# Kernel optimization log

Hardware: AMD Instinct MI355X
Metric: run time of the kernel (lower is better)

The kernel has to match this reference:

```python
import jax, jax.numpy as jnp
import numpy as np
from jax import lax

WORD_NUM = 30000
EMBED = 128
RNN = 256
CLASSES = 9
BATCH = 128
SEQ = 512


def setup_inputs() -> dict:
    key = jax.random.key(0)
    ks = jax.random.split(key, 7)
    s_e = 1.0 / np.sqrt(EMBED)
    s_r = 1.0 / np.sqrt(RNN)
    return {
        "input_x": jax.random.randint(ks[0], (BATCH, SEQ), 0, WORD_NUM, dtype=jnp.int32),
        "embed": jax.random.normal(ks[1], (WORD_NUM, EMBED), dtype=jnp.float32) * 0.05,
        # LSTM kernel/recurrent kernel, gate order i|f|g|o (Keras convention)
        "W": jax.random.normal(ks[2], (EMBED, 4 * RNN), dtype=jnp.float32) * s_e,
        "U": jax.random.normal(ks[3], (RNN, 4 * RNN), dtype=jnp.float32) * s_r,
        "b": jnp.zeros((4 * RNN,), dtype=jnp.float32),
        "Wout": jax.random.normal(ks[4], (RNN, CLASSES), dtype=jnp.float32) * s_r,
        "bout": jnp.zeros((CLASSES,), dtype=jnp.float32),
    }


def _lstm(xs, W, U, b, h0, c0):
    # xs: [T, B, E] -> hidden sequence [T, B, R], final (h, c)
    def step(carry, x):
        h, c = carry
        z = x @ W + h @ U + b  # [B, 4R]
        i, f, g, o = jnp.split(z, 4, axis=-1)
        i = jax.nn.sigmoid(i)
        f = jax.nn.sigmoid(f)
        g = jnp.tanh(g)
        o = jax.nn.sigmoid(o)
        c = f * c + i * g
        h = o * jnp.tanh(c)
        return (h, c), h

    (h, c), hs = lax.scan(step, (h0, c0), xs)
    return hs, h, c


def reference(input_x, embed, W, U, b, Wout, bout):
    # Embedding lookup: [B, S] -> [B, S, E]
    x = embed[input_x]
    B = x.shape[0]
    R = U.shape[0]
    h0 = jnp.zeros((B, R), dtype=x.dtype)
    c0 = jnp.zeros((B, R), dtype=x.dtype)
    xs = jnp.swapaxes(x, 0, 1)  # [S, B, E] for time-major scan
    hs, h_last, c_last = _lstm(xs, W, U, b, h0, c0)
    hs = jnp.swapaxes(hs, 0, 1)  # [B, S, R]
    probs = jax.nn.softmax(hs @ Wout + bout, axis=-1)  # [B, S, C]
    # Keras return_state -> (sequence_output, last_h, last_c); state=(hc, hs)
    return probs, (h_last, c_last)
```

## Files before the change

### kernel.cpp

```cpp
#include <hip/hip_runtime.h>
#include <math.h>

#define B 128
#define S 512
#define E 128
#define R 256

#define NG 32
#define QW 8
#define ELS 4
#define OUTS 128
#define UNITS 32

typedef float v2f __attribute__((ext_vector_type(2)));

static const size_t HX_OFF   = 0;
static const size_t XG_OFF   = HX_OFF + 2ull * B * R;
static const size_t WUT_OFF  = XG_OFF + (size_t)S * B * E;
static const size_t SYNC_OFF = WUT_OFF + 1024ull * 384;
static const size_t WS_FLOATS = SYNC_OFF + 1024;

#define HOUT_OFF 589824
#define COUT_OFF 622592

__global__ void zero_sync(int* __restrict__ sync) {
    sync[threadIdx.x] = 0;
}

__global__ void gather_x(const int* __restrict__ idx, const float* __restrict__ embed,
                         float* __restrict__ Xg) {
    int t    = blockIdx.x;
    int tid  = threadIdx.x;
    int b    = tid >> 1;
    int half = tid & 1;
    int row  = idx[(size_t)b * S + t];
    const float4* er = (const float4*)(embed + (size_t)row * E) + half * 16;
    float4* xw = (float4*)(Xg + ((size_t)t * B + b) * E) + half * 16;
#pragma unroll
    for (int k = 0; k < 16; ++k) xw[k] = er[k];
}

__global__ void make_wut(const float* __restrict__ W, const float* __restrict__ U,
                         float* __restrict__ WUt) {
    int j = blockIdx.x;
    int s = threadIdx.x;
    float v = (s < E) ? W[(size_t)s * 1024 + j] : U[(size_t)(s - E) * 1024 + j];
    WUt[(size_t)j * 384 + s] = v;
}

__device__ __forceinline__ float sigm(float x) { return 1.f / (1.f + __expf(-x)); }

__launch_bounds__(512, 2)
__global__ void lstm_persist(const float* __restrict__ Xg, const float* __restrict__ WUt,
                             const float* __restrict__ bias, const float* __restrict__ Wout,
                             const float* __restrict__ bout, float* __restrict__ out,
                             float* __restrict__ HX, int* __restrict__ sync) {
    __shared__ float act[ELS][E + R];
    __shared__ float partial[4][ELS][OUTS];
    __shared__ float woutT[9][260];
    __shared__ float zrow[ELS][12];

    const int tid  = threadIdx.x;
    const int wg   = blockIdx.x;
    const int g    = wg >> 3;
    const int q    = wg & 7;
    const int lane = tid & 63;
    const int wv   = __builtin_amdgcn_readfirstlane(tid >> 6);
    const int ks   = wv >> 1;
    const int oi   = ((wv & 1) << 6) | lane;
    const int j    = (oi >> 5) * 256 + q * 32 + (oi & 31);

    float4 wx[8], wh[16];
    {
        const float4* wrow = (const float4*)(WUt + (size_t)j * 384);
#pragma unroll
        for (int p = 0; p < 8; ++p)  wx[p] = wrow[8 * ks + p];
#pragma unroll
        for (int p = 0; p < 16; ++p) wh[p] = wrow[32 + 16 * ks + p];
    }

    float bias_g0 = 0.f, bias_g1 = 0.f, bias_g2 = 0.f, bias_g3 = 0.f, creg = 0.f;
    if (tid < 128) {
        int u = tid & 31;
        bias_g0 = bias[0 * 256 + q * 32 + u];
        bias_g1 = bias[1 * 256 + q * 32 + u];
        bias_g2 = bias[2 * 256 + q * 32 + u];
        bias_g3 = bias[3 * 256 + q * 32 + u];
    }
    float boutr = 0.f;
    if (wv == 0 && (lane & 15) < 9) boutr = bout[lane & 15];

    for (int i = tid; i < 9 * 256; i += 512) {
        int c = i >> 8, r = i & 255;
        woutT[c][r] = Wout[(size_t)r * 9 + c];
    }
    for (int i = tid; i < ELS * (E + R); i += 512) ((float*)act)[i] = 0.f;
    __syncthreads();
    if (tid < 256) {
        int el = tid >> 6, e2 = (tid & 63) * 2;
        *(v2f*)&act[el][e2] = *(const v2f*)&Xg[((size_t)0 * B + g * 4 + el) * E + e2];
    }
    __syncthreads();

    int* cnt = sync + g * 32;
    int* flg = sync + g * 32 + 16;

    for (int t = 0; t < S; ++t) {
        float ac0 = 0.f, ac1 = 0.f, ac2 = 0.f, ac3 = 0.f;
        {
            const int xo = 32 * ks;
#pragma unroll
            for (int p = 0; p < 8; ++p) {
                float4 w  = wx[p];
                float4 a0 = *(const float4*)&act[0][xo + 4 * p];
                float4 a1 = *(const float4*)&act[1][xo + 4 * p];
                float4 a2 = *(const float4*)&act[2][xo + 4 * p];
                float4 a3 = *(const float4*)&act[3][xo + 4 * p];
                ac0 += w.x * a0.x + w.y * a0.y + w.z * a0.z + w.w * a0.w;
                ac1 += w.x * a1.x + w.y * a1.y + w.z * a1.z + w.w * a1.w;
                ac2 += w.x * a2.x + w.y * a2.y + w.z * a2.z + w.w * a2.w;
                ac3 += w.x * a3.x + w.y * a3.y + w.z * a3.z + w.w * a3.w;
            }
            const int ho = E + 64 * ks;
#pragma unroll
            for (int p = 0; p < 16; ++p) {
                float4 w  = wh[p];
                float4 a0 = *(const float4*)&act[0][ho + 4 * p];
                float4 a1 = *(const float4*)&act[1][ho + 4 * p];
                float4 a2 = *(const float4*)&act[2][ho + 4 * p];
                float4 a3 = *(const float4*)&act[3][ho + 4 * p];
                ac0 += w.x * a0.x + w.y * a0.y + w.z * a0.z + w.w * a0.w;
                ac1 += w.x * a1.x + w.y * a1.y + w.z * a1.z + w.w * a1.w;
                ac2 += w.x * a2.x + w.y * a2.y + w.z * a2.z + w.w * a2.w;
                ac3 += w.x * a3.x + w.y * a3.y + w.z * a3.z + w.w * a3.w;
            }
        }
        partial[ks][0][oi] = ac0;
        partial[ks][1][oi] = ac1;
        partial[ks][2][oi] = ac2;
        partial[ks][3][oi] = ac3;
        __syncthreads();

        if (tid < 128) {
            int el = tid >> 5, u = tid & 31;
            float z0 = bias_g0, z1 = bias_g1, z2 = bias_g2, z3 = bias_g3;
#pragma unroll
            for (int kk = 0; kk < 4; ++kk) {
                z0 += partial[kk][el][0 * 32 + u];
                z1 += partial[kk][el][1 * 32 + u];
                z2 += partial[kk][el][2 * 32 + u];
                z3 += partial[kk][el][3 * 32 + u];
            }
            float ig = sigm(z0), fg = sigm(z1), gv = tanhf(z2), og = sigm(z3);
            creg = fg * creg + ig * gv;
            float h = og * tanhf(creg);
            float* haddr = HX + ((size_t)(t & 1) * B + g * 4 + el) * R + q * 32 + u;
            asm volatile("global_store_dword %0, %1, off sc0 sc1" :: "v"(haddr), "v"(h) : "memory");
            if (t == S - 1) {
                out[HOUT_OFF + (size_t)(g * 4 + el) * R + q * 32 + u] = h;
                out[COUT_OFF + (size_t)(g * 4 + el) * R + q * 32 + u] = creg;
            }
        }
        v2f xpre;
        const bool do_x = (tid < 256) && (t < S - 1);
        if (do_x) {
            int el = tid >> 6, e2 = (tid & 63) * 2;
            xpre = *(const v2f*)&Xg[((size_t)(t + 1) * B + g * 4 + el) * E + e2];
        }
        asm volatile("s_waitcnt vmcnt(0)" ::: "memory");
        __syncthreads();

        if (tid == 0) {
            int epoch = t + 1;
            int old = __hip_atomic_fetch_add(cnt, 1, __ATOMIC_ACQ_REL, __HIP_MEMORY_SCOPE_AGENT);
            if (old == QW - 1) {
                __hip_atomic_store(cnt, 0, __ATOMIC_RELAXED, __HIP_MEMORY_SCOPE_AGENT);
                __hip_atomic_store(flg, epoch, __ATOMIC_RELEASE, __HIP_MEMORY_SCOPE_AGENT);
            } else {
                int it = 0;
                while (__hip_atomic_load(flg, __ATOMIC_RELAXED, __HIP_MEMORY_SCOPE_AGENT) < epoch
                       && ++it < (1 << 16)) {}
            }
        }
        __syncthreads();

        {
            int el = tid >> 7, r2 = (tid & 127) * 2;
            const float* hsrc = HX + ((size_t)(t & 1) * B + g * 4 + el) * R + r2;
            v2f hv;
            asm volatile("global_load_dwordx2 %0, %1, off sc0 sc1" : "=v"(hv) : "v"(hsrc) : "memory");
            asm volatile("s_waitcnt vmcnt(0)" ::: "memory");
            *(v2f*)&act[el][E + r2] = hv;
        }
        if (do_x) {
            int el = tid >> 6, e2 = (tid & 63) * 2;
            *(v2f*)&act[el][e2] = xpre;
        }
        __syncthreads();

        if (q == (t & 7) && wv == 0) {
            int el = lane >> 4, c = lane & 15;
            float z = boutr;
            if (c < 9) {
#pragma unroll 16
                for (int p = 0; p < 64; ++p) {
                    float4 w = *(const float4*)&woutT[c][4 * p];
                    float4 a = *(const float4*)&act[el][E + 4 * p];
                    z += w.x * a.x + w.y * a.y + w.z * a.z + w.w * a.w;
                }
                zrow[el][c] = z;
            }
            asm volatile("s_waitcnt lgkmcnt(0)" ::: "memory");
            if (c < 9) {
                float m = zrow[el][0];
#pragma unroll
                for (int cc = 1; cc < 9; ++cc) m = fmaxf(m, zrow[el][cc]);
                float ssum = 0.f;
#pragma unroll
                for (int cc = 0; cc < 9; ++cc) ssum += __expf(zrow[el][cc] - m);
                out[((size_t)(g * 4 + el) * S + t) * 9 + c] = __expf(z - m) / ssum;
            }
        }
    }
}

extern "C" void kernel_launch(void* const* d_in, const int* in_sizes, int n_in,
                              void* d_out, int out_size, void* d_ws, size_t ws_size,
                              hipStream_t stream) {
    const int*   idx   = (const int*)d_in[0];
    const float* embed = (const float*)d_in[1];
    const float* W     = (const float*)d_in[2];
    const float* U     = (const float*)d_in[3];
    const float* bias  = (const float*)d_in[4];
    const float* Wout  = (const float*)d_in[5];
    const float* bout  = (const float*)d_in[6];
    float*       outp  = (float*)d_out;
    float*       ws    = (float*)d_ws;

    if (ws_size < WS_FLOATS * sizeof(float)) return;

    float* HX   = ws + HX_OFF;
    float* Xg   = ws + XG_OFF;
    float* WUt  = ws + WUT_OFF;
    int*   sy   = (int*)(ws + SYNC_OFF);

    zero_sync<<<1, 1024, 0, stream>>>(sy);
    gather_x<<<S, 256, 0, stream>>>(idx, embed, Xg);
    make_wut<<<1024, 384, 0, stream>>>(W, U, WUt);

    void* args[] = {&Xg, &WUt, &bias, &Wout, &bout, &outp, &HX, &sy};
    (void)hipLaunchCooperativeKernel((const void*)lstm_persist, dim3(256), dim3(512),
                                     args, 0, stream);
}
```

Baseline: 4.639 ms.

## Move output projection and softmax out of recurrent loop into separate kernel

The per-step output projection and softmax, previously run inside the persistent LSTM loop by one workgroup per step, now goes into a separate out_probs kernel. That kernel reads a full hidden-state history buffer written during the recurrence. The x gather is also relaid out to a transposed [t][e4][b] float4 layout, with per-element scalar reads inside the loop. The goal is to shorten the serial critical path of each timestep, at the cost of an extra 64MB hidden-state write plus a read-back pass, and uncoalesced scalar x loads.

```diff
diff --git a/kernel.cpp b/kernel.cpp
--- a/kernel.cpp
+++ b/kernel.cpp
@@ -10,15 +10,15 @@
 #define QW 8
 #define ELS 4
 #define OUTS 128
-#define UNITS 32
 
 typedef float v2f __attribute__((ext_vector_type(2)));
 
 static const size_t HX_OFF   = 0;
-static const size_t XG_OFF   = HX_OFF + 2ull * B * R;
-static const size_t WUT_OFF  = XG_OFF + (size_t)S * B * E;
-static const size_t SYNC_OFF = WUT_OFF + 1024ull * 384;
-static const size_t WS_FLOATS = SYNC_OFF + 1024;
+static const size_t SYNC_OFF = HX_OFF + 2ull * B * R;
+static const size_t XG_OFF   = SYNC_OFF + 1024;
+static const size_t HS_OFF   = XG_OFF + (size_t)S * E * B;
+static const size_t WUT_OFF  = HS_OFF + (size_t)S * B * R;
+static const size_t WS_FLOATS = WUT_OFF + 1024ull * 384;
 
 #define HOUT_OFF 589824
 #define COUT_OFF 622592
@@ -28,16 +28,19 @@
 }
 
 __global__ void gather_x(const int* __restrict__ idx, const float* __restrict__ embed,
-                         float* __restrict__ Xg) {
+                         float4* __restrict__ X4) {
     int t    = blockIdx.x;
     int tid  = threadIdx.x;
-    int b    = tid >> 1;
-    int half = tid & 1;
+    int b    = tid & 127;
+    int half = tid >> 7;
     int row  = idx[(size_t)b * S + t];
-    const float4* er = (const float4*)(embed + (size_t)row * E) + half * 16;
-    float4* xw = (float4*)(Xg + ((size_t)t * B + b) * E) + half * 16;
-#pragma unroll
-    for (int k = 0; k < 16; ++k) xw[k] = er[k];
+    const float4* er = (const float4*)embed + (size_t)row * (E / 4);
+    size_t xbase = (size_t)t * (E / 4) * B + b;
+#pragma unroll
+    for (int kk = 0; kk < 16; ++kk) {
+        int e4 = half * 16 + kk;
+        X4[xbase + (size_t)e4 * B] = er[e4];
+    }
 }
 
 __global__ void make_wut(const float* __restrict__ W, const float* __restrict__ U,
@@ -51,14 +54,12 @@
 __device__ __forceinline__ float sigm(float x) { return 1.f / (1.f + __expf(-x)); }
 
 __launch_bounds__(512, 2)
-__global__ void lstm_persist(const float* __restrict__ Xg, const float* __restrict__ WUt,
-                             const float* __restrict__ bias, const float* __restrict__ Wout,
-                             const float* __restrict__ bout, float* __restrict__ out,
-                             float* __restrict__ HX, int* __restrict__ sync) {
+__global__ void lstm_persist(const float4* __restrict__ Xg, const float* __restrict__ WUt,
+                             const float* __restrict__ bias, float* __restrict__ out,
+                             float* __restrict__ HX, float* __restrict__ HS,
+                             int* __restrict__ sync) {
     __shared__ float act[ELS][E + R];
     __shared__ float partial[4][ELS][OUTS];
-    __shared__ float woutT[9][260];
-    __shared__ float zrow[ELS][12];
 
     const int tid  = threadIdx.x;
     const int wg   = blockIdx.x;
@@ -87,18 +88,17 @@
         bias_g2 = bias[2 * 256 + q * 32 + u];
         bias_g3 = bias[3 * 256 + q * 32 + u];
     }
-    float boutr = 0.f;
-    if (wv == 0 && (lane & 15) < 9) boutr = bout[lane & 15];
-
-    for (int i = tid; i < 9 * 256; i += 512) {
-        int c = i >> 8, r = i & 255;
-        woutT[c][r] = Wout[(size_t)r * 9 + c];
-    }
+
     for (int i = tid; i < ELS * (E + R); i += 512) ((float*)act)[i] = 0.f;
     __syncthreads();
     if (tid < 256) {
         int el = tid >> 6, e2 = (tid & 63) * 2;
-        *(v2f*)&act[el][e2] = *(const v2f*)&Xg[((size_t)0 * B + g * 4 + el) * E + e2];
+        const float* xsrc = (const float*)(Xg + (size_t)0 * (E / 4) * B);
+        float x0 = ((const float*)&Xg[((size_t)(e2 >> 2)) * B + (4 * g + el)])[e2 & 3];
+        float x1 = ((const float*)&Xg[((size_t)((e2 + 1) >> 2)) * B + (4 * g + el)])[(e2 + 1) & 3];
+        act[el][e2] = x0;
+        act[el][e2 + 1] = x1;
+        (void)xsrc;
     }
     __syncthreads();
 
@@ -154,18 +154,23 @@
             float ig = sigm(z0), fg = sigm(z1), gv = tanhf(z2), og = sigm(z3);
             creg = fg * creg + ig * gv;
             float h = og * tanhf(creg);
-            float* haddr = HX + ((size_t)(t & 1) * B + g * 4 + el) * R + q * 32 + u;
+            int brow = 4 * g + el, rr = q * 32 + u;
+            HS[(size_t)t * B * R + (size_t)brow * R + rr] = h;
+            float* haddr = HX + ((size_t)(t & 1) * B + brow) * R + rr;
             asm volatile("global_store_dword %0, %1, off sc0 sc1" :: "v"(haddr), "v"(h) : "memory");
             if (t == S - 1) {
-                out[HOUT_OFF + (size_t)(g * 4 + el) * R + q * 32 + u] = h;
-                out[COUT_OFF + (size_t)(g * 4 + el) * R + q * 32 + u] = creg;
+                out[HOUT_OFF + (size_t)brow * R + rr] = h;
+                out[COUT_OFF + (size_t)brow * R + rr] = creg;
             }
         }
         v2f xpre;
         const bool do_x = (tid < 256) && (t < S - 1);
         if (do_x) {
             int el = tid >> 6, e2 = (tid & 63) * 2;
-            xpre = *(const v2f*)&Xg[((size_t)(t + 1) * B + g * 4 + el) * E + e2];
+            xpre.x = ((const float*)&Xg[(size_t)(t + 1) * (E / 4) * B
+                                        + ((size_t)(e2 >> 2)) * B + (4 * g + el)])[e2 & 3];
+            xpre.y = ((const float*)&Xg[(size_t)(t + 1) * (E / 4) * B
+                                        + ((size_t)((e2 + 1) >> 2)) * B + (4 * g + el)])[(e2 + 1) & 3];
         }
         asm volatile("s_waitcnt vmcnt(0)" ::: "memory");
         __syncthreads();
@@ -186,10 +191,11 @@
 
         {
             int el = tid >> 7, r2 = (tid & 127) * 2;
-            const float* hsrc = HX + ((size_t)(t & 1) * B + g * 4 + el) * R + r2;
+            const float* hsrc = HX + ((size_t)(t & 1) * B + 4 * g + el) * R + r2;
             v2f hv;
-            asm volatile("global_load_dwordx2 %0, %1, off sc0 sc1" : "=v"(hv) : "v"(hsrc) : "memory");
-            asm volatile("s_waitcnt vmcnt(0)" ::: "memory");
+            asm volatile("global_load_dwordx2 %0, %1, off sc0 sc1\n\t"
+                         "s_waitcnt vmcnt(0)"
+                         : "=&v"(hv) : "v"(hsrc) : "memory");
             *(v2f*)&act[el][E + r2] = hv;
         }
         if (do_x) {
@@ -197,31 +203,41 @@
             *(v2f*)&act[el][e2] = xpre;
         }
         __syncthreads();
-
-        if (q == (t & 7) && wv == 0) {
-            int el = lane >> 4, c = lane & 15;
-            float z = boutr;
-            if (c < 9) {
-#pragma unroll 16
-                for (int p = 0; p < 64; ++p) {
-                    float4 w = *(const float4*)&woutT[c][4 * p];
-                    float4 a = *(const float4*)&act[el][E + 4 * p];
-                    z += w.x * a.x + w.y * a.y + w.z * a.z + w.w * a.w;
-                }
-                zrow[el][c] = z;
-            }
-            asm volatile("s_waitcnt lgkmcnt(0)" ::: "memory");
-            if (c < 9) {
-                float m = zrow[el][0];
-#pragma unroll
-                for (int cc = 1; cc < 9; ++cc) m = fmaxf(m, zrow[el][cc]);
-                float ssum = 0.f;
-#pragma unroll
-                for (int cc = 0; cc < 9; ++cc) ssum += __expf(zrow[el][cc] - m);
-                out[((size_t)(g * 4 + el) * S + t) * 9 + c] = __expf(z - m) / ssum;
-            }
-        }
-    }
+    }
+}
+
+__global__ void out_probs(const float* __restrict__ HS, const float* __restrict__ Wout,
+                          const float* __restrict__ bout, float* __restrict__ out) {
+    __shared__ float woutT[9][260];
+    int t    = blockIdx.x;
+    int bg   = blockIdx.y;
+    int lane = threadIdx.x;
+    int b    = bg * 64 + lane;
+    for (int i = lane; i < 9 * 256; i += 64)
+        woutT[i >> 8][i & 255] = Wout[(size_t)(i & 255) * 9 + (i >> 8)];
+    __syncthreads();
+    float acc[9];
+#pragma unroll
+    for (int c = 0; c < 9; ++c) acc[c] = bout[c];
+    const float4* hrow = (const float4*)(HS + (size_t)t * B * R + (size_t)b * R);
+#pragma unroll 8
+    for (int r4 = 0; r4 < 64; ++r4) {
+        float4 hv = hrow[r4];
+#pragma unroll
+        for (int c = 0; c < 9; ++c) {
+            float4 wv = *(const float4*)&woutT[c][4 * r4];
+            acc[c] += hv.x * wv.x + hv.y * wv.y + hv.z * wv.z + hv.w * wv.w;
+        }
+    }
+    float m = acc[0];
+#pragma unroll
+    for (int c = 1; c < 9; ++c) m = fmaxf(m, acc[c]);
+    float e[9], sum = 0.f;
+#pragma unroll
+    for (int c = 0; c < 9; ++c) { e[c] = __expf(acc[c] - m); sum += e[c]; }
+    float inv = 1.f / sum;
+#pragma unroll
+    for (int c = 0; c < 9; ++c) out[((size_t)b * S + t) * 9 + c] = e[c] * inv;
 }
 
 extern "C" void kernel_launch(void* const* d_in, const int* in_sizes, int n_in,
@@ -239,16 +255,20 @@
 
     if (ws_size < WS_FLOATS * sizeof(float)) return;
 
-    float* HX   = ws + HX_OFF;
-    float* Xg   = ws + XG_OFF;
-    float* WUt  = ws + WUT_OFF;
-    int*   sy   = (int*)(ws + SYNC_OFF);
+    float*  HX   = ws + HX_OFF;
+    int*    sy   = (int*)(ws + SYNC_OFF);
+    float4* Xg   = (float4*)(ws + XG_OFF);
+    float*  HS   = ws + HS_OFF;
+    float*  WUt  = ws + WUT_OFF;
 
     zero_sync<<<1, 1024, 0, stream>>>(sy);
     gather_x<<<S, 256, 0, stream>>>(idx, embed, Xg);
     make_wut<<<1024, 384, 0, stream>>>(W, U, WUt);
 
-    void* args[] = {&Xg, &WUt, &bias, &Wout, &bout, &outp, &HX, &sy};
+    void* args[] = {(void*)&Xg, (void*)&WUt, (void*)&bias, (void*)&outp,
+                    (void*)&HX, (void*)&HS, (void*)&sy};
     (void)hipLaunchCooperativeKernel((const void*)lstm_persist, dim3(256), dim3(512),
                                      args, 0, stream);
-}
+
+    out_probs<<<dim3(S, 2), 64, 0, stream>>>(HS, Wout, bout, outp);
+}
```

New measurement: 5.203 ms. 1.12x slower.
